# Kernel optimization log

Hardware: AMD Instinct MI355X
Metric: run time of the kernel (lower is better)

Reference implementation:

```python
import jax, jax.numpy as jnp
import numpy as np

V, E, H, O, T = 50000, 300, 512, 64, 21
B, S = 256, 128


def setup_inputs() -> dict:
    key = jax.random.key(0)
    ks = jax.random.split(key, 20)
    u = lambda k, shape, s: jax.random.uniform(k, shape, jnp.float32, -s, s)
    sg = 1.0 / np.sqrt(H)
    s2 = 1.0 / np.sqrt(2 * H)
    return {
        "x": jax.random.randint(ks[0], (B, S), 0, V),
        "ner_tags": jax.random.randint(ks[1], (B, S), 0, T),
        "mask": jnp.ones((B, S), dtype=bool),
        "emb": jax.random.normal(ks[2], (V, E), jnp.float32) * 0.1,
        "W_ih_f": u(ks[3], (3 * H, E), sg),
        "W_hh_f": u(ks[4], (3 * H, H), sg),
        "b_ih_f": u(ks[5], (3 * H,), sg),
        "b_hh_f": u(ks[6], (3 * H,), sg),
        "W_ih_b": u(ks[7], (3 * H, E), sg),
        "W_hh_b": u(ks[8], (3 * H, H), sg),
        "b_ih_b": u(ks[9], (3 * H,), sg),
        "b_hh_b": u(ks[10], (3 * H,), sg),
        "attn_w": u(ks[11], (1, 2 * H), s2),
        "attn_b": u(ks[12], (1,), s2),
        "fc_w": u(ks[13], (O, 2 * H), s2),
        "fc_b": u(ks[14], (O,), s2),
        "ner_w": u(ks[15], (T, 2 * H), s2),
        "ner_b": u(ks[16], (T,), s2),
        "crf_start": u(ks[17], (T,), 0.1),
        "crf_end": u(ks[18], (T,), 0.1),
        "crf_trans": u(ks[19], (T, T), 0.1),
    }


def _gru_dir(xp, h0, W_hh, b_hh, reverse):
    # xp: [S, B, 3H] precomputed input projections (PyTorch GRU gate order r,z,n)
    def step(h, xpt):
        hp = h @ W_hh.T + b_hh
        xr, xz, xn = jnp.split(xpt, 3, axis=-1)
        hr, hz, hn = jnp.split(hp, 3, axis=-1)
        r = jax.nn.sigmoid(xr + hr)
        z = jax.nn.sigmoid(xz + hz)
        n = jnp.tanh(xn + r * hn)
        h_new = (1.0 - z) * n + z * h
        return h_new, h_new
    _, hs = jax.lax.scan(step, h0, xp, reverse=reverse)
    return hs  # [S, B, H]


def _crf_nll(emissions, tags, mask, start, end, trans):
    # emissions: [B, S, T]; torchcrf forward algorithm, reduction='mean'
    dt = emissions.dtype
    em_t = jnp.transpose(emissions, (1, 0, 2))        # [S, B, T]
    m_t = jnp.transpose(mask, (1, 0))                  # [S, B]

    def step(score, inp):
        em, m = inp
        # [B,T,1] + [1,T,T] + [B,1,T] -> logsumexp over prev tag
        ns = jax.nn.logsumexp(score[:, :, None] + trans[None] + em[:, None, :], axis=1)
        score = jnp.where(m[:, None], ns, score)
        return score, None

    score0 = start[None, :] + em_t[0]
    score, _ = jax.lax.scan(step, score0, (em_t[1:], m_t[1:]))
    logZ = jax.nn.logsumexp(score + end[None, :], axis=1)  # [B]

    mf = mask.astype(dt)
    em_sc = jnp.take_along_axis(emissions, tags[..., None], axis=2)[..., 0]  # [B,S]
    tr_sc = trans[tags[:, :-1], tags[:, 1:]]                                  # [B,S-1]
    seq_ends = jnp.sum(mask, axis=1).astype(jnp.int32) - 1
    last_tags = jnp.take_along_axis(tags, seq_ends[:, None].astype(tags.dtype), axis=1)[:, 0]
    num = (start[tags[:, 0]] + em_sc[:, 0]
           + jnp.sum((em_sc[:, 1:] + tr_sc) * mf[:, 1:], axis=1)
           + end[last_tags])
    return -jnp.mean(num - logZ)


def _forward(x, ner_tags, mask, emb,
             W_ih_f, W_hh_f, b_ih_f, b_hh_f,
             W_ih_b, W_hh_b, b_ih_b, b_hh_b,
             attn_w, attn_b, fc_w, fc_b, ner_w, ner_b,
             crf_start, crf_end, crf_trans):
    b = x.shape[0]
    xe = emb[x]                                  # [B,S,E]
    xs = jnp.transpose(xe, (1, 0, 2))            # [S,B,E]
    h0 = jnp.zeros((b, H), dtype=emb.dtype)
    xpf = jnp.einsum('sbe,ge->sbg', xs, W_ih_f) + b_ih_f
    hf = _gru_dir(xpf, h0, W_hh_f, b_hh_f, False)
    xpb = jnp.einsum('sbe,ge->sbg', xs, W_ih_b) + b_ih_b
    hb = _gru_dir(xpb, h0, W_hh_b, b_hh_b, True)
    gru_out = jnp.transpose(jnp.concatenate([hf, hb], axis=-1), (1, 0, 2))  # [B,S,2H]

    # attention pooling over seq dim (no masking, as in original)
    scores = gru_out @ attn_w.T + attn_b          # [B,S,1]
    w = jax.nn.softmax(scores, axis=1)
    ctx = jnp.sum(w * gru_out, axis=1)            # [B,2H]
    intent_logits = ctx @ fc_w.T + fc_b           # [B,O]  (dropout = identity in eval)

    emissions = gru_out @ ner_w.T + ner_b         # [B,S,T]
    ner_loss = _crf_nll(emissions, ner_tags, mask, crf_start, crf_end, crf_trans)
    return intent_logits, ner_loss


def reference(x, ner_tags, mask, emb,
              W_ih_f, W_hh_f, b_ih_f, b_hh_f,
              W_ih_b, W_hh_b, b_ih_b, b_hh_b,
              attn_w, attn_b, fc_w, fc_b, ner_w, ner_b,
              crf_start, crf_end, crf_trans):
    return _forward(x, ner_tags, mask, emb,
                    W_ih_f, W_hh_f, b_ih_f, b_hh_f,
                    W_ih_b, W_hh_b, b_ih_b, b_hh_b,
                    attn_w, attn_b, fc_w, fc_b, ner_w, ner_b,
                    crf_start, crf_end, crf_trans)
```

## Files before the change

### kernel.cpp

```cpp
#include <hip/hip_runtime.h>
#include <hip/hip_cooperative_groups.h>
#include <stdint.h>

namespace cg = cooperative_groups;

typedef __attribute__((ext_vector_type(8))) short s8_t;
typedef __attribute__((ext_vector_type(4))) short s4v_t;
typedef __attribute__((ext_vector_type(4))) float f4_t;
typedef unsigned short u16;

#define V_  50000
#define E_  300
#define EP_ 320
#define H_  512
#define G_  1536
#define O_  64
#define T_  21
#define B_  256
#define S_  128
#define BS_ 32768

__device__ __forceinline__ float b2f(u16 u) {
    union { unsigned int u; float f; } v; v.u = ((unsigned int)u) << 16; return v.f;
}
__device__ __forceinline__ u16 f2b(float f) {
    union { float f; unsigned int u; } v; v.f = f;
    unsigned int r = v.u + 0x7fffu + ((v.u >> 16) & 1u);
    return (u16)(r >> 16);
}
__device__ __forceinline__ float fsig(float x) {
    return __builtin_amdgcn_rcpf(1.f + __expf(-x));
}
__device__ __forceinline__ float ftanh(float x) {
    return 1.f - 2.f * __builtin_amdgcn_rcpf(1.f + __expf(2.f * x));
}

__global__ void prep_kernel(const float* wih_f, const float* wih_b,
                            const float* whh_f, const float* whh_b,
                            const float* ner_w,
                            u16* wih_bf, u16* whh_bf, u16* nerw_bf)
{
    const int NW = 3072 * EP_;
    const int NH = 2 * G_ * H_;
    const int NN = 32 * 1024;
    int stride = gridDim.x * blockDim.x;
    for (int i = blockIdx.x * blockDim.x + threadIdx.x; i < NW + NH + NN; i += stride) {
        if (i < NW) {
            int n = i / EP_, k = i % EP_;
            float v = 0.f;
            if (k < E_) v = (n < G_) ? wih_f[n * E_ + k] : wih_b[(n - G_) * E_ + k];
            wih_bf[i] = f2b(v);
        } else if (i < NW + NH) {
            int j = i - NW;
            int d = j / (G_ * H_), r = j % (G_ * H_);
            whh_bf[j] = f2b(d == 0 ? whh_f[r] : whh_b[r]);
        } else {
            int j = i - NW - NH;
            int t = j / 1024, k = j % 1024;
            nerw_bf[j] = f2b(t < T_ ? ner_w[t * 1024 + k] : 0.f);
        }
    }
}

__global__ void gather_kernel(const int* x, const float* emb, u16* xe)
{
    int stride = gridDim.x * blockDim.x;
    for (int i = blockIdx.x * blockDim.x + threadIdx.x; i < BS_ * EP_; i += stride) {
        int m = i / EP_, k = i % EP_;
        int s = m >> 8, b = m & 255;
        float v = 0.f;
        if (k < E_) v = emb[(size_t)x[b * S_ + s] * E_ + k];
        xe[i] = f2b(v);
    }
}

#define XST 328
__global__ __launch_bounds__(256, 2) void gru_persist(
    const u16* __restrict__ xe, const u16* __restrict__ wih,
    const float* bih_f, const float* bih_b,
    const u16* __restrict__ whh_bf,
    const float* bhh_f, const float* bhh_b,
    u16* h_hi, unsigned int* flag, unsigned int* xcnt)
{
    __shared__ u16 sWx[48 * XST];
    __shared__ f4_t red[4][2][64];
    __shared__ unsigned int role_sh[2];

    cg::grid_group grid = cg::this_grid();
    int tid = threadIdx.x, l = tid & 63, wid = tid >> 6;

    if (tid == 0) {
        unsigned int xcc = __builtin_amdgcn_s_getreg((7u << 11) | 20u) & 7u;
        unsigned int slot = __hip_atomic_fetch_add(&xcnt[xcc], 1u,
                                __ATOMIC_RELAXED, __HIP_MEMORY_SCOPE_AGENT);
        role_sh[0] = xcc; role_sh[1] = slot;
    }
    grid.sync();
    bool fast = true;
    for (int i = 0; i < 8; ++i)
        fast = fast && (__hip_atomic_load(&xcnt[i], __ATOMIC_RELAXED,
                            __HIP_MEMORY_SCOPE_AGENT) == 64u);
    int g, hs;
    if (fast) {
        unsigned int xcc = role_sh[0], slot = role_sh[1];
        g  = (int)(xcc * 2 + (slot >> 5));
        hs = (int)(slot & 31);
    } else {
        g = blockIdx.x >> 5; hs = blockIdx.x & 31;
    }
    int dir = g >> 3, bt = g & 7;
    int wpair = wid & 1;
    int khi   = wid >> 1;
    int r0  = bt * 32 + wpair * 16;
    int hc0 = hs * 16;
    int lr = l & 15, lk = (l >> 4) * 8;
    int koff_h = khi ? 256 : 0;
    int koff_x = khi ? 160 : 0;

    for (int idx = tid; idx < 48 * 40; idx += 256) {
        int rr = idx / 40, ck = (idx % 40) * 8;
        int gcol = (rr >> 4) * H_ + hc0 + (rr & 15);
        size_t goff = ((size_t)dir * G_ + gcol) * (size_t)EP_ + ck;
        *(s8_t*)&sWx[rr * XST + ck] = *(const s8_t*)&wih[goff];
    }

    s8_t Bh[3][8];
#pragma unroll
    for (int c = 0; c < 3; ++c)
#pragma unroll
        for (int kk = 0; kk < 8; ++kk)
            Bh[c][kk] = *(const s8_t*)&whh_bf[
                ((size_t)dir * G_ + c * H_ + hc0 + lr) * (size_t)H_ + koff_h + lk + kk * 32];
    __syncthreads();

    int lc = l & 15, lr4 = (l >> 4) * 4;
    int hc = hc0 + lc;
    const float* bih = dir ? bih_b : bih_f;
    const float* bhh = dir ? bhh_b : bhh_f;
    float br  = bih[hc] + bhh[hc];
    float bz  = bih[H_ + hc] + bhh[H_ + hc];
    float bxn = bih[2 * H_ + hc];
    float bhn = bhh[2 * H_ + hc];
    float hstate[4] = {0.f, 0.f, 0.f, 0.f};

    f4_t xac[3];
    auto xgemm = [&](int ttx) {
#pragma unroll
        for (int c = 0; c < 3; ++c) xac[c] = (f4_t){0.f, 0.f, 0.f, 0.f};
        const u16* xp = xe + ((size_t)ttx * B_ + r0 + lr) * EP_ + koff_x + lk;
#pragma unroll
        for (int kk = 0; kk < 5; ++kk) {
            s8_t ax = *(const s8_t*)(xp + kk * 32);
#pragma unroll
            for (int c = 0; c < 3; ++c) {
                s8_t bx = *(const s8_t*)&sWx[(c * 16 + lr) * XST + koff_x + lk + kk * 32];
                xac[c] = __builtin_amdgcn_mfma_f32_16x16x32_bf16(ax, bx, xac[c], 0, 0, 0);
            }
        }
    };

    xgemm(dir ? (S_ - 1) : 0);

#pragma unroll 1
    for (int t = 0; t < S_; ++t) {
        int tt = dir ? (S_ - 1 - t) : t;

        if (t > 0) {
            if (fast) {
                const unsigned int* fp = flag + g * 32 + khi * 16 + (l & 15);
                unsigned int tgt = (unsigned int)t;
                int spin = 0;
                for (;;) {
                    unsigned int v = tgt;
                    if (l < 16) v = __hip_atomic_load(fp, __ATOMIC_RELAXED,
                                                      __HIP_MEMORY_SCOPE_AGENT);
                    if (__all((int)(v >= tgt))) break;
                    if (++spin > 2) __builtin_amdgcn_s_sleep(1);
                }
                asm volatile("" ::: "memory");
            } else {
                __threadfence();
                grid.sync();
                __threadfence();
            }
        }

        f4_t ahn = {0.f, 0.f, 0.f, 0.f};
        if (t > 0) {
            int prev = dir ? (tt + 1) : (tt - 1);
            const u16* hb = h_hi + ((size_t)dir * S_ + prev) * B_ * H_
                                 + (size_t)(r0 + lr) * H_ + koff_h + lk;
            s8_t ah[8];
#pragma unroll
            for (int kk = 0; kk < 8; ++kk) ah[kk] = *(const s8_t*)(hb + kk * 32);
#pragma unroll
            for (int kk = 0; kk < 8; ++kk) {
                xac[0] = __builtin_amdgcn_mfma_f32_16x16x32_bf16(ah[kk], Bh[0][kk], xac[0], 0, 0, 0);
                xac[1] = __builtin_amdgcn_mfma_f32_16x16x32_bf16(ah[kk], Bh[1][kk], xac[1], 0, 0, 0);
                ahn    = __builtin_amdgcn_mfma_f32_16x16x32_bf16(ah[kk], Bh[2][kk], ahn,    0, 0, 0);
            }
        }

        if (khi) {
            red[0][wpair][l] = xac[0];
            red[1][wpair][l] = xac[1];
            red[2][wpair][l] = xac[2];
            red[3][wpair][l] = ahn;
        }
        __syncthreads();
        if (!khi) {
            f4_t q0 = red[0][wpair][l];
            f4_t q1 = red[1][wpair][l];
            f4_t q2 = red[2][wpair][l];
            f4_t q3 = red[3][wpair][l];
            u16* hw = h_hi + ((size_t)dir * S_ + tt) * B_ * H_;
#pragma unroll
            for (int r = 0; r < 4; ++r) {
                int row = r0 + lr4 + r;
                float pre_r = xac[0][r] + q0[r] + br;
                float pre_z = xac[1][r] + q1[r] + bz;
                float xn  = xac[2][r] + q2[r] + bxn;
                float hnv = ahn[r] + q3[r] + bhn;
                float rg = fsig(pre_r);
                float zg = fsig(pre_z);
                float ng = ftanh(xn + rg * hnv);
                float hnew = (1.f - zg) * ng + zg * hstate[r];
                hstate[r] = hnew;
                hw[(size_t)row * H_ + hc] = f2b(hnew);
            }
        }

        __syncthreads();
        if (t < S_ - 1) {
            if (fast && tid == 0)
                __hip_atomic_store(flag + g * 32 + hs, (unsigned int)(t + 1),
                                   __ATOMIC_RELAXED, __HIP_MEMORY_SCOPE_AGENT);
            xgemm(dir ? (S_ - 2 - t) : (t + 1));
        }
    }
}

__global__ __launch_bounds__(256) void scores_kernel(const u16* h_hi, const float* attn_w,
                                                     const float* attn_b, float* scores)
{
    int wid = threadIdx.x >> 6, l = threadIdx.x & 63;
    int row = blockIdx.x * 4 + wid;
    int dir = l >> 5;
    int hc = (l & 31) * 16;
    const u16* hp = h_hi + (size_t)dir * BS_ * H_ + (size_t)row * H_ + hc;
    s8_t v0 = *(const s8_t*)(hp);
    s8_t v1 = *(const s8_t*)(hp + 8);
    const float* aw = attn_w + dir * H_ + hc;
    float acc = 0.f;
#pragma unroll
    for (int j = 0; j < 8; ++j) acc += b2f((u16)v0[j]) * aw[j];
#pragma unroll
    for (int j = 0; j < 8; ++j) acc += b2f((u16)v1[j]) * aw[8 + j];
    for (int off = 32; off; off >>= 1) acc += __shfl_down(acc, off);
    if (l == 0) {
        int s = row >> 8, b = row & 255;
        scores[b * S_ + s] = acc + attn_b[0];
    }
}

__global__ __launch_bounds__(256) void attnctx_kernel(const u16* h_hi, const float* scores,
                                                      float* ctx)
{
    __shared__ float sc[S_];
    __shared__ float tmp[S_];
    int b = blockIdx.x, tid = threadIdx.x;
    if (tid < S_) sc[tid] = scores[b * S_ + tid];
    __syncthreads();
    if (tid < S_) tmp[tid] = sc[tid];
    __syncthreads();
    for (int st = 64; st > 0; st >>= 1) {
        if (tid < st) tmp[tid] = fmaxf(tmp[tid], tmp[tid + st]);
        __syncthreads();
    }
    float mx = tmp[0];
    __syncthreads();
    if (tid < S_) { sc[tid] = __expf(sc[tid] - mx); tmp[tid] = sc[tid]; }
    __syncthreads();
    for (int st = 64; st > 0; st >>= 1) {
        if (tid < st) tmp[tid] += tmp[tid + st];
        __syncthreads();
    }
    float inv = 1.f / tmp[0];
    __syncthreads();
    if (tid < S_) sc[tid] *= inv;
    __syncthreads();

    int c = tid * 4;
    int dir = c >> 9, hcv = c & (H_ - 1);
    const u16* hp = h_hi + (size_t)dir * BS_ * H_;
    float a0 = 0, a1 = 0, a2 = 0, a3 = 0;
    for (int s = 0; s < S_; ++s) {
        float w = sc[s];
        s4v_t v = *(const s4v_t*)(hp + ((size_t)s * B_ + b) * H_ + hcv);
        a0 += w * b2f((u16)v[0]); a1 += w * b2f((u16)v[1]);
        a2 += w * b2f((u16)v[2]); a3 += w * b2f((u16)v[3]);
    }
    float* cp = ctx + (size_t)b * 1024 + c;
    cp[0] = a0; cp[1] = a1; cp[2] = a2; cp[3] = a3;
}

__global__ __launch_bounds__(256) void intent_kernel(const float* ctx, const float* fc_w,
                                                     const float* fc_b, float* out)
{
    __shared__ float cs[1024];
    int b = blockIdx.x, tid = threadIdx.x;
    for (int i = tid; i < 1024; i += 256) cs[i] = ctx[(size_t)b * 1024 + i];
    __syncthreads();
    if (tid < O_) {
        float acc = fc_b[tid];
        const float* w = fc_w + (size_t)tid * 1024;
        for (int k = 0; k < 1024; ++k) acc += cs[k] * w[k];
        out[b * O_ + tid] = acc;
    }
}

__global__ __launch_bounds__(256) void emis_kernel(const u16* h_hi, const u16* nerw,
                                                   const float* ner_b, float* em)
{
    int tid = threadIdx.x, l = tid & 63, wid = tid >> 6;
    int rb = blockIdx.x * 64 + wid * 16;
    int lr = l & 15, lk = (l >> 4) * 8;
    f4_t acc[2] = {};
    for (int kk = 0; kk < 32; ++kk) {
        int k0 = kk * 32 + lk;
        int dir = k0 >> 9, hcv = k0 & (H_ - 1);
        s8_t a  = *(const s8_t*)(h_hi + (size_t)dir * BS_ * H_ + (size_t)(rb + lr) * H_ + hcv);
        s8_t b0 = *(const s8_t*)(nerw + (size_t)lr * 1024 + k0);
        s8_t b1 = *(const s8_t*)(nerw + (size_t)(16 + lr) * 1024 + k0);
        acc[0] = __builtin_amdgcn_mfma_f32_16x16x32_bf16(a, b0, acc[0], 0, 0, 0);
        acc[1] = __builtin_amdgcn_mfma_f32_16x16x32_bf16(a, b1, acc[1], 0, 0, 0);
    }
    int lc = l & 15, lr4 = (l >> 4) * 4;
#pragma unroll
    for (int f = 0; f < 2; ++f) {
        int tcol = f * 16 + lc;
        if (tcol < T_) {
            float nb = ner_b[tcol];
#pragma unroll
            for (int r = 0; r < 4; ++r) {
                int row = rb + lr4 + r;
                int s = row >> 8, bb = row & 255;
                em[((size_t)bb * S_ + s) * T_ + tcol] = acc[f][r] + nb;
            }
        }
    }
}

__global__ __launch_bounds__(64) void num_kernel(const int* tags, const float* em,
                                                 const float* cstart, const float* cend,
                                                 const float* ctrans, float* numv)
{
    int b = blockIdx.x, l = threadIdx.x;
    const int* tg = tags + b * S_;
    float acc = 0.f;
#pragma unroll
    for (int q = 0; q < 2; ++q) {
        int s = l + q * 64;
        int tc = tg[s];
        acc += em[((size_t)b * S_ + s) * T_ + tc];
        if (s > 0) acc += ctrans[tg[s - 1] * T_ + tc];
    }
#pragma unroll
    for (int off = 32; off; off >>= 1) acc += __shfl_down(acc, off);
    if (l == 0) numv[b] = acc + cstart[tg[0]] + cend[tg[S_ - 1]];
}

__global__ __launch_bounds__(64) void crf2_kernel(const float* em, const float* cstart,
                                                  const float* cend, const float* ctrans,
                                                  float* logZ)
{
    int b = blockIdx.x, l = threadIdx.x;
    bool act = l < T_;
    float E[T_];
#pragma unroll
    for (int i = 0; i < T_; ++i) E[i] = act ? __expf(ctrans[i * T_ + l]) : 0.f;
    const float* eb = em + (size_t)b * S_ * T_;
    float sc = act ? (cstart[l] + eb[l]) : -1e30f;
#pragma unroll 1
    for (int s = 1; s < S_; ++s) {
        float emv = act ? eb[s * T_ + l] : 0.f;
        float m = sc;
#pragma unroll
        for (int off = 16; off; off >>= 1) m = fmaxf(m, __shfl_xor(m, off, 32));
        float e = act ? __expf(sc - m) : 0.f;
        float sum = 0.f;
#pragma unroll
        for (int i = 0; i < T_; ++i) sum += __shfl(e, i, 32) * E[i];
        sc = act ? (m + __logf(sum) + emv) : -1e30f;
    }
    float fin = act ? (sc + cend[l]) : -1e30f;
    float m = fin;
#pragma unroll
    for (int off = 16; off; off >>= 1) m = fmaxf(m, __shfl_xor(m, off, 32));
    float z = act ? __expf(fin - m) : 0.f;
#pragma unroll
    for (int off = 16; off; off >>= 1) z += __shfl_xor(z, off, 32);
    if (l == 0) logZ[b] = m + __logf(z);
}

__global__ __launch_bounds__(256) void loss_kernel(const float* numv, const float* logZ,
                                                   float* out)
{
    __shared__ float red[B_];
    int t = threadIdx.x;
    red[t] = numv[t] - logZ[t];
    __syncthreads();
    for (int st = 128; st > 0; st >>= 1) {
        if (t < st) red[t] += red[t + st];
        __syncthreads();
    }
    if (t == 0) out[16384] = -red[0] / (float)B_;
}

extern "C" void kernel_launch(void* const* d_in, const int* in_sizes, int n_in,
                              void* d_out, int out_size, void* d_ws, size_t ws_size,
                              hipStream_t stream)
{
    const int*   x      = (const int*)  d_in[0];
    const int*   tags   = (const int*)  d_in[1];
    const float* emb    = (const float*)d_in[3];
    const float* wih_f  = (const float*)d_in[4];
    const float* whh_f  = (const float*)d_in[5];
    const float* bih_f  = (const float*)d_in[6];
    const float* bhh_f  = (const float*)d_in[7];
    const float* wih_b  = (const float*)d_in[8];
    const float* whh_b  = (const float*)d_in[9];
    const float* bih_b  = (const float*)d_in[10];
    const float* bhh_b  = (const float*)d_in[11];
    const float* attn_w = (const float*)d_in[12];
    const float* attn_b = (const float*)d_in[13];
    const float* fc_w   = (const float*)d_in[14];
    const float* fc_b   = (const float*)d_in[15];
    const float* ner_w  = (const float*)d_in[16];
    const float* ner_b  = (const float*)d_in[17];
    const float* cstart = (const float*)d_in[18];
    const float* cend   = (const float*)d_in[19];
    const float* ctrans = (const float*)d_in[20];
    float* out = (float*)d_out;

    char* p = (char*)d_ws;
    auto alloc = [&](size_t bytes) { void* r = (void*)p; p += (bytes + 255) & ~(size_t)255; return r; };
    u16* wih_bf  = (u16*)alloc((size_t)3072 * EP_ * 2);
    u16* whh_bf  = (u16*)alloc((size_t)2 * G_ * H_ * 2);
    u16* nerw_bf = (u16*)alloc((size_t)32 * 1024 * 2);
    u16* xe      = (u16*)alloc((size_t)BS_ * EP_ * 2);
    u16* h_hi    = (u16*)alloc((size_t)2 * BS_ * H_ * 2);
    unsigned int* flag = (unsigned int*)alloc(16 * 32 * 4);
    unsigned int* xcnt = (unsigned int*)alloc(64);
    float* scores= (float*)alloc((size_t)BS_ * 4);
    float* ctx   = (float*)alloc((size_t)B_ * 1024 * 4);
    float* em    = (float*)alloc((size_t)B_ * S_ * T_ * 4);
    float* numv  = (float*)alloc(1024);
    float* logZ  = (float*)alloc(1024);

    hipMemsetAsync(flag, 0, 16 * 32 * 4, stream);
    hipMemsetAsync(xcnt, 0, 64, stream);

    hipLaunchKernelGGL(prep_kernel, dim3(2048), dim3(256), 0, stream,
                       wih_f, wih_b, whh_f, whh_b, ner_w, wih_bf, whh_bf, nerw_bf);
    hipLaunchKernelGGL(gather_kernel, dim3(4096), dim3(256), 0, stream, x, emb, xe);

    void* args[] = { &xe, &wih_bf, &bih_f, &bih_b, &whh_bf, &bhh_f, &bhh_b,
                     &h_hi, &flag, &xcnt };
    hipLaunchCooperativeKernel((const void*)gru_persist, dim3(512), dim3(256), args, 0, stream);

    hipLaunchKernelGGL(scores_kernel, dim3(BS_ / 4), dim3(256), 0, stream,
                       h_hi, attn_w, attn_b, scores);
    hipLaunchKernelGGL(attnctx_kernel, dim3(B_), dim3(256), 0, stream, h_hi, scores, ctx);
    hipLaunchKernelGGL(intent_kernel, dim3(B_), dim3(256), 0, stream, ctx, fc_w, fc_b, out);
    hipLaunchKernelGGL(emis_kernel, dim3(BS_ / 64), dim3(256), 0, stream, h_hi, nerw_bf, ner_b, em);
    hipLaunchKernelGGL(num_kernel, dim3(B_), dim3(64), 0, stream, tags, em, cstart, cend, ctrans, numv);
    hipLaunchKernelGGL(crf2_kernel, dim3(B_), dim3(64), 0, stream, em, cstart, cend, ctrans, logZ);
    hipLaunchKernelGGL(loss_kernel, dim3(1), dim3(256), 0, stream, numv, logZ, out);
}
```

Baseline: 808.2 us.

## Tile hidden-state layout, fuse scores into emission pass, vectorize embedding gather

Stores GRU hidden states in a column-tiled layout [dir][s][c/16][b][16], so that the per-step h writes and the recurrent A-operand loads touch contiguous 16-column chunks. The attention score dot product is folded into the emission MFMA kernel, so h is read once for both. The embedding gather now converts 8 elements per thread with float4 loads. Reads in attnctx become more strided, and the gru_persist index math changes.

```diff
diff --git a/kernel.cpp b/kernel.cpp
--- a/kernel.cpp
+++ b/kernel.cpp
@@ -19,6 +19,10 @@
 #define B_  256
 #define S_  128
 #define BS_ 32768
+
+__device__ __forceinline__ size_t hidx(int dir, int s, int c, int b) {
+    return ((((size_t)dir * S_ + s) * 32 + (c >> 4)) * B_ + b) * 16 + (c & 15);
+}
 
 __device__ __forceinline__ float b2f(u16 u) {
     union { unsigned int u; float f; } v; v.u = ((unsigned int)u) << 16; return v.f;
@@ -65,12 +69,27 @@
 __global__ void gather_kernel(const int* x, const float* emb, u16* xe)
 {
     int stride = gridDim.x * blockDim.x;
-    for (int i = blockIdx.x * blockDim.x + threadIdx.x; i < BS_ * EP_; i += stride) {
-        int m = i / EP_, k = i % EP_;
+    const int NU = BS_ * 40;
+    for (int u = blockIdx.x * blockDim.x + threadIdx.x; u < NU; u += stride) {
+        int m = u / 40, k8 = u % 40;
+        int k = k8 * 8;
         int s = m >> 8, b = m & 255;
-        float v = 0.f;
-        if (k < E_) v = emb[(size_t)x[b * S_ + s] * E_ + k];
-        xe[i] = f2b(v);
+        short out[8];
+        if (k + 8 <= E_) {
+            const float* ep = emb + (size_t)x[b * S_ + s] * E_ + k;
+            float4 f0 = *(const float4*)(ep);
+            float4 f1 = *(const float4*)(ep + 4);
+            out[0] = (short)f2b(f0.x); out[1] = (short)f2b(f0.y);
+            out[2] = (short)f2b(f0.z); out[3] = (short)f2b(f0.w);
+            out[4] = (short)f2b(f1.x); out[5] = (short)f2b(f1.y);
+            out[6] = (short)f2b(f1.z); out[7] = (short)f2b(f1.w);
+        } else {
+            const float* ep = emb + (size_t)x[b * S_ + s] * E_;
+#pragma unroll
+            for (int j = 0; j < 8; ++j)
+                out[j] = (short)f2b((k + j < E_) ? ep[k + j] : 0.f);
+        }
+        *(s8_t*)(xe + (size_t)m * EP_ + k) = *(s8_t*)out;
     }
 }
 
@@ -188,11 +207,11 @@
         f4_t ahn = {0.f, 0.f, 0.f, 0.f};
         if (t > 0) {
             int prev = dir ? (tt + 1) : (tt - 1);
-            const u16* hb = h_hi + ((size_t)dir * S_ + prev) * B_ * H_
-                                 + (size_t)(r0 + lr) * H_ + koff_h + lk;
+            const u16* hb = h_hi + hidx(dir, prev, koff_h + lk, r0 + lr);
             s8_t ah[8];
 #pragma unroll
-            for (int kk = 0; kk < 8; ++kk) ah[kk] = *(const s8_t*)(hb + kk * 32);
+            for (int kk = 0; kk < 8; ++kk)
+                ah[kk] = *(const s8_t*)(hb + (size_t)kk * 2 * B_ * 16);
 #pragma unroll
             for (int kk = 0; kk < 8; ++kk) {
                 xac[0] = __builtin_amdgcn_mfma_f32_16x16x32_bf16(ah[kk], Bh[0][kk], xac[0], 0, 0, 0);
@@ -213,7 +232,7 @@
             f4_t q1 = red[1][wpair][l];
             f4_t q2 = red[2][wpair][l];
             f4_t q3 = red[3][wpair][l];
-            u16* hw = h_hi + ((size_t)dir * S_ + tt) * B_ * H_;
+            u16* hw = h_hi + hidx(dir, tt, hc0 + lc, 0);
 #pragma unroll
             for (int r = 0; r < 4; ++r) {
                 int row = r0 + lr4 + r;
@@ -226,7 +245,7 @@
                 float ng = ftanh(xn + rg * hnv);
                 float hnew = (1.f - zg) * ng + zg * hstate[r];
                 hstate[r] = hnew;
-                hw[(size_t)row * H_ + hc] = f2b(hnew);
+                hw[(size_t)row * 16] = f2b(hnew);
             }
         }
 
@@ -240,26 +259,51 @@
     }
 }
 
-__global__ __launch_bounds__(256) void scores_kernel(const u16* h_hi, const float* attn_w,
-                                                     const float* attn_b, float* scores)
-{
-    int wid = threadIdx.x >> 6, l = threadIdx.x & 63;
-    int row = blockIdx.x * 4 + wid;
-    int dir = l >> 5;
-    int hc = (l & 31) * 16;
-    const u16* hp = h_hi + (size_t)dir * BS_ * H_ + (size_t)row * H_ + hc;
-    s8_t v0 = *(const s8_t*)(hp);
-    s8_t v1 = *(const s8_t*)(hp + 8);
-    const float* aw = attn_w + dir * H_ + hc;
-    float acc = 0.f;
-#pragma unroll
-    for (int j = 0; j < 8; ++j) acc += b2f((u16)v0[j]) * aw[j];
-#pragma unroll
-    for (int j = 0; j < 8; ++j) acc += b2f((u16)v1[j]) * aw[8 + j];
-    for (int off = 32; off; off >>= 1) acc += __shfl_down(acc, off);
-    if (l == 0) {
-        int s = row >> 8, b = row & 255;
-        scores[b * S_ + s] = acc + attn_b[0];
+__global__ __launch_bounds__(256) void rowpass_kernel(const u16* h_hi, const u16* nerw,
+                                                      const float* ner_b,
+                                                      const float* attn_w, const float* attn_b,
+                                                      float* em, float* scores)
+{
+    int tid = threadIdx.x, l = tid & 63, wid = tid >> 6;
+    int rb = blockIdx.x * 64 + wid * 16;
+    int lr = l & 15, lk = (l >> 4) * 8;
+    f4_t acc[2] = {};
+    float sacc = 0.f;
+    for (int kk = 0; kk < 32; ++kk) {
+        int k0 = kk * 32 + lk;
+        int dir = k0 >> 9, c = k0 & 511;
+        int row = rb + lr;
+        s8_t a = *(const s8_t*)(h_hi + hidx(dir, row >> 8, c, row & 255));
+        s8_t b0 = *(const s8_t*)(nerw + (size_t)lr * 1024 + k0);
+        s8_t b1 = *(const s8_t*)(nerw + (size_t)(16 + lr) * 1024 + k0);
+        acc[0] = __builtin_amdgcn_mfma_f32_16x16x32_bf16(a, b0, acc[0], 0, 0, 0);
+        acc[1] = __builtin_amdgcn_mfma_f32_16x16x32_bf16(a, b1, acc[1], 0, 0, 0);
+        float4 aw0 = *(const float4*)(attn_w + k0);
+        float4 aw1 = *(const float4*)(attn_w + k0 + 4);
+        sacc += b2f((u16)a[0]) * aw0.x + b2f((u16)a[1]) * aw0.y
+              + b2f((u16)a[2]) * aw0.z + b2f((u16)a[3]) * aw0.w
+              + b2f((u16)a[4]) * aw1.x + b2f((u16)a[5]) * aw1.y
+              + b2f((u16)a[6]) * aw1.z + b2f((u16)a[7]) * aw1.w;
+    }
+    sacc += __shfl_down(sacc, 32);
+    sacc += __shfl_down(sacc, 16);
+    if (l < 16) {
+        int row = rb + l;
+        scores[(row & 255) * S_ + (row >> 8)] = sacc + attn_b[0];
+    }
+    int lc = l & 15, lr4 = (l >> 4) * 4;
+#pragma unroll
+    for (int f = 0; f < 2; ++f) {
+        int tcol = f * 16 + lc;
+        if (tcol < T_) {
+            float nb = ner_b[tcol];
+#pragma unroll
+            for (int r = 0; r < 4; ++r) {
+                int row = rb + lr4 + r;
+                int s = row >> 8, bb = row & 255;
+                em[((size_t)bb * S_ + s) * T_ + tcol] = acc[f][r] + nb;
+            }
+        }
     }
 }
 
@@ -291,12 +335,11 @@
     __syncthreads();
 
     int c = tid * 4;
-    int dir = c >> 9, hcv = c & (H_ - 1);
-    const u16* hp = h_hi + (size_t)dir * BS_ * H_;
+    int dir = c >> 9, hcv = c & 511;
     float a0 = 0, a1 = 0, a2 = 0, a3 = 0;
     for (int s = 0; s < S_; ++s) {
         float w = sc[s];
-        s4v_t v = *(const s4v_t*)(hp + ((size_t)s * B_ + b) * H_ + hcv);
+        s4v_t v = *(const s4v_t*)(h_hi + hidx(dir, s, hcv, b));
         a0 += w * b2f((u16)v[0]); a1 += w * b2f((u16)v[1]);
         a2 += w * b2f((u16)v[2]); a3 += w * b2f((u16)v[3]);
     }
@@ -316,38 +359,6 @@
         const float* w = fc_w + (size_t)tid * 1024;
         for (int k = 0; k < 1024; ++k) acc += cs[k] * w[k];
         out[b * O_ + tid] = acc;
-    }
-}
-
-__global__ __launch_bounds__(256) void emis_kernel(const u16* h_hi, const u16* nerw,
-                                                   const float* ner_b, float* em)
-{
-    int tid = threadIdx.x, l = tid & 63, wid = tid >> 6;
-    int rb = blockIdx.x * 64 + wid * 16;
-    int lr = l & 15, lk = (l >> 4) * 8;
-    f4_t acc[2] = {};
-    for (int kk = 0; kk < 32; ++kk) {
-        int k0 = kk * 32 + lk;
-        int dir = k0 >> 9, hcv = k0 & (H_ - 1);
-        s8_t a  = *(const s8_t*)(h_hi + (size_t)dir * BS_ * H_ + (size_t)(rb + lr) * H_ + hcv);
-        s8_t b0 = *(const s8_t*)(nerw + (size_t)lr * 1024 + k0);
-        s8_t b1 = *(const s8_t*)(nerw + (size_t)(16 + lr) * 1024 + k0);
-        acc[0] = __builtin_amdgcn_mfma_f32_16x16x32_bf16(a, b0, acc[0], 0, 0, 0);
-        acc[1] = __builtin_amdgcn_mfma_f32_16x16x32_bf16(a, b1, acc[1], 0, 0, 0);
-    }
-    int lc = l & 15, lr4 = (l >> 4) * 4;
-#pragma unroll
-    for (int f = 0; f < 2; ++f) {
-        int tcol = f * 16 + lc;
-        if (tcol < T_) {
-            float nb = ner_b[tcol];
-#pragma unroll
-            for (int r = 0; r < 4; ++r) {
-                int row = rb + lr4 + r;
-                int s = row >> 8, bb = row & 255;
-                em[((size_t)bb * S_ + s) * T_ + tcol] = acc[f][r] + nb;
-            }
-        }
     }
 }
 
@@ -463,17 +474,16 @@
 
     hipLaunchKernelGGL(prep_kernel, dim3(2048), dim3(256), 0, stream,
                        wih_f, wih_b, whh_f, whh_b, ner_w, wih_bf, whh_bf, nerw_bf);
-    hipLaunchKernelGGL(gather_kernel, dim3(4096), dim3(256), 0, stream, x, emb, xe);
+    hipLaunchKernelGGL(gather_kernel, dim3(2048), dim3(256), 0, stream, x, emb, xe);
 
     void* args[] = { &xe, &wih_bf, &bih_f, &bih_b, &whh_bf, &bhh_f, &bhh_b,
                      &h_hi, &flag, &xcnt };
     hipLaunchCooperativeKernel((const void*)gru_persist, dim3(512), dim3(256), args, 0, stream);
 
-    hipLaunchKernelGGL(scores_kernel, dim3(BS_ / 4), dim3(256), 0, stream,
-                       h_hi, attn_w, attn_b, scores);
+    hipLaunchKernelGGL(rowpass_kernel, dim3(BS_ / 64), dim3(256), 0, stream,
+                       h_hi, nerw_bf, ner_b, attn_w, attn_b, em, scores);
     hipLaunchKernelGGL(attnctx_kernel, dim3(B_), dim3(256), 0, stream, h_hi, scores, ctx);
     hipLaunchKernelGGL(intent_kernel, dim3(B_), dim3(256), 0, stream, ctx, fc_w, fc_b, out);
-    hipLaunchKernelGGL(emis_kernel, dim3(BS_ / 64), dim3(256), 0, stream, h_hi, nerw_bf, ner_b, em);
     hipLaunchKernelGGL(num_kernel, dim3(B_), dim3(64), 0, stream, tags, em, cstart, cend, ctrans, numv);
     hipLaunchKernelGGL(crf2_kernel, dim3(B_), dim3(64), 0, stream, em, cstart, cend, ctrans, logZ);
     hipLaunchKernelGGL(loss_kernel, dim3(1), dim3(256), 0, stream, numv, logZ, out);
```

Result: faster. 770.2 us (-4.7%).
